# Kernel optimization log

Measured on AMD Instinct MI355X. Metric: run time of the kernel, lower is better.

## Reference

```python
import jax, jax.numpy as jnp
from jax import lax
import numpy as np

DIM = 384
NUM_HEADS = 8
HEAD_DIM = DIM // NUM_HEADS


def setup_inputs() -> dict:
    key = jax.random.key(0)
    k_x, k_qw, k_qb, k_lw, k_lb = jax.random.split(key, 5)
    B, H, W = 2, 64, 64
    N = H * W
    x = jax.random.normal(k_x, (B, N, DIM), dtype=jnp.float32)
    # nn.Linear(dim, 3*dim): weight (3C, C), bias (3C,)
    qkv_w = jax.random.normal(k_qw, (3 * DIM, DIM), dtype=jnp.float32) * (1.0 / np.sqrt(DIM))
    qkv_b = jax.random.normal(k_qb, (3 * DIM,), dtype=jnp.float32) * 0.02
    # nn.Conv2d(dim, dim, 3, padding=1, groups=dim): weight (C, 1, 3, 3), bias (C,)
    lepe_w = jax.random.normal(k_lw, (DIM, 1, 3, 3), dtype=jnp.float32) * (1.0 / 3.0)
    lepe_b = jax.random.normal(k_lb, (DIM,), dtype=jnp.float32) * 0.02
    return {"x": x, "qkv_w": qkv_w, "qkv_b": qkv_b, "lepe_w": lepe_w, "lepe_b": lepe_b, "H": H, "W": W}


def reference(x, qkv_w, qkv_b, lepe_w, lepe_b, H, W):
    B, N, C = x.shape
    hd = C // NUM_HEADS
    scale = hd ** -0.5
    # qkv projection: (B, N, 3C) -> (B, N, 3, heads, head_dim)
    qkv = (jnp.einsum('bnc,oc->bno', x, qkv_w) + qkv_b).reshape(B, N, 3, NUM_HEADS, hd)
    q, k, v = qkv[:, :, 0], qkv[:, :, 1], qkv[:, :, 2]  # each (B, N, heads, hd)
    attn = jnp.einsum('bnhd,bmhd->bhnm', q * scale, k)   # (B, heads, N, N)
    attn = jax.nn.softmax(attn, axis=-1)
    out = jnp.einsum('bhnm,bmhd->bnhd', attn, v).reshape(B, N, C)
    # LePE: depthwise 3x3 conv on v in NCHW layout
    v_img = v.reshape(B, H, W, C).transpose(0, 3, 1, 2)  # (B, C, H, W)
    lepe = lax.conv_general_dilated(
        v_img, lepe_w, window_strides=(1, 1), padding='SAME',
        feature_group_count=C,
        dimension_numbers=('NCHW', 'OIHW', 'NCHW'))
    lepe = lepe + lepe_b[None, :, None, None]
    return out + lepe.transpose(0, 2, 3, 1).reshape(B, N, C)
```

## Files before the change

kernel.cpp:

```cpp
#include <hip/hip_runtime.h>
#include <stdint.h>

#define DIM   384
#define NH    8
#define HD    48
#define NTOK  4096
#define KDIM  384
#define SCALEL2E 0.20823509610f

typedef float  f32x4   __attribute__((ext_vector_type(4)));
typedef float  f32x16  __attribute__((ext_vector_type(16)));
typedef __bf16 bf16x8  __attribute__((ext_vector_type(8)));

#if __has_builtin(__builtin_amdgcn_exp2f)
#define EXP2F(x) __builtin_amdgcn_exp2f(x)
#else
#define EXP2F(x) exp2f(x)
#endif

__device__ __forceinline__ unsigned short f2bf(float f) {
  union { float f; unsigned int u; } c; c.f = f;
  unsigned int r = (c.u + 0x7FFFu + ((c.u >> 16) & 1u)) >> 16;
  return (unsigned short)r;
}
__device__ __forceinline__ float bf2f(unsigned short h) {
  union { unsigned int u; float f; } c; c.u = ((unsigned int)h) << 16;
  return c.f;
}


__global__ void prep_kernel(const float* __restrict__ x, const float* __restrict__ w,
                            unsigned short* __restrict__ x_bf,
                            unsigned short* __restrict__ w_bf) {
  int tid = blockIdx.x * blockDim.x + threadIdx.x;
  int stride = gridDim.x * blockDim.x;
  for (int i = tid; i < 786432; i += stride) {
    float4 v = ((const float4*)x)[i];
    ushort4 o;
    o.x = f2bf(v.x); o.y = f2bf(v.y); o.z = f2bf(v.z); o.w = f2bf(v.w);
    ((ushort4*)x_bf)[i] = o;
  }
  for (int i = tid; i < 110592; i += stride) {
    float4 v = ((const float4*)w)[i];
    ushort4 o;
    o.x = f2bf(v.x); o.y = f2bf(v.y); o.z = f2bf(v.z); o.w = f2bf(v.w);
    ((ushort4*)w_bf)[i] = o;
  }
}

__global__ __launch_bounds__(256) void qkv_gemm(
    const unsigned short* __restrict__ A,
    const unsigned short* __restrict__ Bw,
    const float* __restrict__ bias,
    unsigned short* __restrict__ qc,
    unsigned short* __restrict__ kc,
    unsigned short* __restrict__ v_t) {
  __shared__ unsigned short ldsA[128 * 32];
  __shared__ unsigned short ldsB[64 * 32];
  __shared__ unsigned short ebuf[64 * 72];
  const int tid = threadIdx.x;
  const int wv = tid >> 6, ln = tid & 63;
  const int lrow = ln & 15, lq = ln >> 4;
  const int m0 = blockIdx.x * 128;
  const int n0 = blockIdx.y * 64;
  const int wm = (wv >> 1) * 64, wn = (wv & 1) * 32;

  f32x4 acc[4][2];
#pragma unroll
  for (int mi = 0; mi < 4; ++mi)
#pragma unroll
    for (int ni = 0; ni < 2; ++ni)
#pragma unroll
      for (int r = 0; r < 4; ++r) acc[mi][ni][r] = 0.f;

  for (int k0 = 0; k0 < KDIM; k0 += 32) {
    __syncthreads();
#pragma unroll
    for (int j = 0; j < 2; ++j) {
      int r16 = wv * 2 + j;
      const unsigned short* ga = A + (size_t)(m0 + r16 * 16 + (ln >> 2)) * KDIM
                                   + k0 + (ln & 3) * 8;
      __builtin_amdgcn_global_load_lds(
          (const __attribute__((address_space(1))) void*)ga,
          (__attribute__((address_space(3))) void*)&ldsA[r16 * 512], 16, 0, 0);
    }
    const unsigned short* gb = Bw + (size_t)(n0 + wv * 16 + (ln >> 2)) * KDIM
                                  + k0 + (ln & 3) * 8;
    __builtin_amdgcn_global_load_lds(
        (const __attribute__((address_space(1))) void*)gb,
        (__attribute__((address_space(3))) void*)&ldsB[wv * 512], 16, 0, 0);
    __syncthreads();
    bf16x8 af[4], bfv[2];
#pragma unroll
    for (int mi = 0; mi < 4; ++mi)
      af[mi] = *(const bf16x8*)&ldsA[(wm + mi * 16 + lrow) * 32 + lq * 8];
#pragma unroll
    for (int ni = 0; ni < 2; ++ni)
      bfv[ni] = *(const bf16x8*)&ldsB[(wn + ni * 16 + lrow) * 32 + lq * 8];
#pragma unroll
    for (int mi = 0; mi < 4; ++mi)
#pragma unroll
      for (int ni = 0; ni < 2; ++ni)
        acc[mi][ni] = __builtin_amdgcn_mfma_f32_16x16x32_bf16(
            af[mi], bfv[ni], acc[mi][ni], 0, 0, 0);
  }

  const int region = (n0 >= 768) ? 2 : (n0 >= 384 ? 1 : 0);
  const float scl = (region == 0) ? SCALEL2E : 1.0f;
  const float bias0 = bias[n0 + wn + lrow];
  const float bias1 = bias[n0 + wn + 16 + lrow];

#pragma unroll
  for (int half = 0; half < 2; ++half) {
    __syncthreads();
    if ((wv >> 1) == half) {
#pragma unroll
      for (int mi = 0; mi < 4; ++mi)
#pragma unroll
        for (int ni = 0; ni < 2; ++ni)
#pragma unroll
          for (int r = 0; r < 4; ++r) {
            int row = mi * 16 + lq * 4 + r;
            int col = wn + ni * 16 + lrow;
            float val = (acc[mi][ni][r] + (ni ? bias1 : bias0)) * scl;
            ebuf[row * 72 + col] = f2bf(val);
          }
    }
    __syncthreads();
    if (region < 2) {
      unsigned short* dst = (region == 0) ? qc : kc;
      const int obase = n0 - region * 384;
#pragma unroll
      for (int i = 0; i < 2; ++i) {
        int id = tid + i * 256;
        int row = id >> 3, cc = id & 7;
        uint4 val = *(const uint4*)&ebuf[row * 72 + cc * 8];
        int nrow = m0 + half * 64 + row;
        int b = nrow >> 12, nn = nrow & 4095;
        int o = obase + cc * 8;
        int h = o / 48, d = o - h * 48;
        *(uint4*)&dst[((size_t)(b * 8 + h) * NTOK + nn) * HD + d] = val;
      }
    } else {
#pragma unroll
      for (int i = 0; i < 2; ++i) {
        int id = tid + i * 256;
        int col = id & 63, rc = id >> 6;
        int r0 = rc * 8;
        union { unsigned short s[8]; uint4 u; } pk;
#pragma unroll
        for (int j = 0; j < 8; ++j)
          pk.s[j] = ebuf[(r0 + j) * 72 + col];
        int nrow = m0 + half * 64 + r0;
        int b = nrow >> 12;
        int o = n0 - 768 + col;
        *(uint4*)&v_t[((size_t)(b * DIM + o)) * NTOK + (nrow & 4095)] = pk.u;
      }
    }
  }
}

__global__ __launch_bounds__(256, 4) void attn_kernel(
    const unsigned short* __restrict__ qc,
    const unsigned short* __restrict__ kcg,
    const unsigned short* __restrict__ v_t,
    const float* __restrict__ lw, const float* __restrict__ lb,
    float* __restrict__ out) {
  __shared__ __align__(16) char smem[33280];
  unsigned short* Kl = (unsigned short*)smem;
  unsigned short* Vl = (unsigned short*)(smem + 16384);
  float* Lsum = (float*)(smem + 32768);
  float* Ol   = (float*)smem;

  const int tid = threadIdx.x;
  const int wv = tid >> 6, ln = tid & 63;
  const int kh = wv >> 1;
  const int wq = wv & 1;
  const int l31 = ln & 31, hh = ln >> 5;
  const int th = tid & 127;
  const int qb = blockIdx.x, bh = blockIdx.y;
  const int b = bh >> 3, hd = bh & 7;

  unsigned short* Kh = Kl + kh * 4096;
  unsigned short* Vh = Vl + kh * 4096;

  int kro[3], kgo[3], vro[3], vgo[3];
#pragma unroll
  for (int i = 0; i < 3; ++i) {
    int idx = th + i * 128;
    int r = idx / 6, cc = idx - r * 6;
    kro[i] = r * 64 + ((cc ^ (r & 7)) * 8);
    kgo[i] = r * 48 + cc * 8;
    int vd = idx >> 3, vc = idx & 7;
    vro[i] = vd * 64 + ((vc ^ (vd & 7)) * 8);
    vgo[i] = vd * 4096 + vc * 8;
  }

  if (th < 8) {
    uint4 one4 = make_uint4(0x3F803F80u, 0x3F803F80u, 0x3F803F80u, 0x3F803F80u);
    *(uint4*)&Vh[3072 + th * 8] = one4;
  }

  const int qrb_self = wq * 32 + l31;
  const unsigned short* qp = qc + ((size_t)bh * NTOK + qb * 64 + qrb_self) * HD + hh * 8;
  bf16x8 Qf[3];
#pragma unroll
  for (int hs = 0; hs < 3; ++hs)
    Qf[hs] = *(const bf16x8*)(qp + hs * 16);

  f32x16 Oacc[2];
#pragma unroll
  for (int dc = 0; dc < 2; ++dc)
#pragma unroll
    for (int r = 0; r < 16; ++r) Oacc[dc][r] = 0.f;

  const unsigned short* kbase = kcg + (size_t)bh * NTOK * HD;
  const unsigned short* vbase = v_t + ((size_t)b * DIM + hd * HD) * NTOK;

  for (int it = 0; it < 32; ++it) {
    const int kt = kh * 32 + it;
    __syncthreads();
    const unsigned short* kg = kbase + (size_t)kt * 64 * HD;
    const unsigned short* vg = vbase + kt * 64;
#pragma unroll
    for (int i = 0; i < 3; ++i) {
      *(uint4*)&Kh[kro[i]] = *(const uint4*)(kg + kgo[i]);
      *(uint4*)&Vh[vro[i]] = *(const uint4*)(vg + vgo[i]);
    }
    __syncthreads();

    unsigned int P32[16];
#pragma unroll
    for (int C = 0; C < 2; ++C) {
      f32x16 s;
#pragma unroll
      for (int r = 0; r < 16; ++r) s[r] = 0.f;
      const int krow = C * 32 + l31;
      const unsigned short* kr = &Kh[krow * 64];
      const int rx = krow & 7;
#pragma unroll
      for (int hs = 0; hs < 3; ++hs) {
        bf16x8 kf = *(const bf16x8*)&kr[((hs * 2 + hh) ^ rx) * 8];
        s = __builtin_amdgcn_mfma_f32_32x32x16_bf16(kf, Qf[hs], s, 0, 0, 0);
      }
#pragma unroll
      for (int t8 = 0; t8 < 8; ++t8) {
        float e0 = EXP2F(s[2 * t8]);
        float e1 = EXP2F(s[2 * t8 + 1]);
        P32[C * 8 + t8] = __builtin_amdgcn_perm(
            __float_as_uint(e1), __float_as_uint(e0), 0x07060302u);
      }
    }

#pragma unroll
    for (int s4 = 0; s4 < 4; ++s4) {
      const int o = (s4 >> 1) * 8 + (s4 & 1) * 4;
      unsigned int send1 = hh ? P32[o + 0] : P32[o + 2];
      unsigned int send2 = hh ? P32[o + 1] : P32[o + 3];
      unsigned int recv1 = (unsigned int)__shfl_xor((int)send1, 32, 64);
      unsigned int recv2 = (unsigned int)__shfl_xor((int)send2, 32, 64);
      union { unsigned int u[4]; bf16x8 v; } pa;
      pa.u[0] = hh ? recv1 : P32[o + 0];
      pa.u[1] = hh ? recv2 : P32[o + 1];
      pa.u[2] = hh ? P32[o + 2] : recv1;
      pa.u[3] = hh ? P32[o + 3] : recv2;
#pragma unroll
      for (int dc = 0; dc < 2; ++dc) {
        int vrow = dc * 32 + l31;
        bf16x8 vf = *(const bf16x8*)&Vh[vrow * 64 + (((s4 * 2 + hh) ^ (vrow & 7)) * 8)];
        Oacc[dc] = __builtin_amdgcn_mfma_f32_32x32x16_bf16(pa.v, vf, Oacc[dc], 0, 0, 0);
      }
    }
  }

  __syncthreads();
  if (l31 == 16) {
#pragma unroll
    for (int r = 0; r < 16; ++r) {
      int qrb = wq * 32 + (r & 3) + 8 * (r >> 2) + 4 * hh;
      Lsum[kh * 64 + qrb] = Oacc[1][r];
    }
  }
  {
    const int px = tid & 63;
    const int c0 = (tid >> 6) * 12;
    const int y = qb;
    const unsigned short* vpl = v_t + ((size_t)b * DIM + hd * HD) * NTOK;
    for (int cj = 0; cj < 12; ++cj) {
      int c = c0 + cj;
      const float* wp = lw + (size_t)(hd * HD + c) * 9;
      float a = lb[hd * HD + c];
      const unsigned short* pl = vpl + (size_t)c * NTOK + y * 64 + px;
#pragma unroll
      for (int dy = -1; dy <= 1; ++dy) {
        if ((unsigned)(y + dy) < 64u) {
#pragma unroll
          for (int dx = -1; dx <= 1; ++dx) {
            if ((unsigned)(px + dx) < 64u)
              a += wp[(dy + 1) * 3 + (dx + 1)] * bf2f(pl[dy * 64 + dx]);
          }
        }
      }
      Ol[px * 48 + c] = a;
    }
  }
  __syncthreads();
  if (kh == 1) {
#pragma unroll
    for (int r = 0; r < 16; ++r) {
      int qrb = wq * 32 + (r & 3) + 8 * (r >> 2) + 4 * hh;
      float linv = 1.0f / (Lsum[qrb] + Lsum[64 + qrb]);
      Ol[qrb * 48 + l31] += Oacc[0][r] * linv;
      if (l31 < 16) Ol[qrb * 48 + 32 + l31] += Oacc[1][r] * linv;
    }
  }
  __syncthreads();
  if (kh == 0) {
#pragma unroll
    for (int r = 0; r < 16; ++r) {
      int qrb = wq * 32 + (r & 3) + 8 * (r >> 2) + 4 * hh;
      float linv = 1.0f / (Lsum[qrb] + Lsum[64 + qrb]);
      float* op = out + ((size_t)(b * NTOK + qb * 64 + qrb)) * DIM + hd * HD;
      op[l31] = Ol[qrb * 48 + l31] + Oacc[0][r] * linv;
      if (l31 < 16) op[32 + l31] = Ol[qrb * 48 + 32 + l31] + Oacc[1][r] * linv;
    }
  }
}

extern "C" void kernel_launch(void* const* d_in, const int* in_sizes, int n_in,
                              void* d_out, int out_size, void* d_ws, size_t ws_size,
                              hipStream_t stream) {
  const float* x      = (const float*)d_in[0];
  const float* qkv_w  = (const float*)d_in[1];
  const float* qkv_b  = (const float*)d_in[2];
  const float* lepe_w = (const float*)d_in[3];
  const float* lepe_b = (const float*)d_in[4];

  char* ws = (char*)d_ws;
  unsigned short* x_bf = (unsigned short*)(ws);
  unsigned short* w_bf = (unsigned short*)(ws + 6291456);
  unsigned short* qcp  = (unsigned short*)(ws + 7176192);
  unsigned short* kcp  = (unsigned short*)(ws + 13467648);
  unsigned short* v_t  = (unsigned short*)(ws + 19759104);
  float* out = (float*)d_out;

  prep_kernel<<<1024, 256, 0, stream>>>(x, qkv_w, x_bf, w_bf);
  qkv_gemm<<<dim3(64, 18), 256, 0, stream>>>(x_bf, w_bf, qkv_b, qcp, kcp, v_t);
  attn_kernel<<<dim3(64, 16), 256, 0, stream>>>(qcp, kcp, v_t, lepe_w, lepe_b, out);
}
```

Measured before the change: 213.4 us.

## Split LePE into separate kernel and process 128 queries per attention block

The depthwise LePE convolution moves into its own kernel, which stages v rows with halos in shared memory and writes the result straight to out. The attention kernel then adds its normalized output onto that. Each attention block now handles two 64-query sets, so every K/V tile loaded into shared memory is reused twice. This halves the grid to 512 blocks and doubles the accumulator registers (launch bounds drop to 2 waves per SIMD). It adds a kernel launch and a read-modify-write of out, and it risks lower occupancy and tail effects.

```diff
diff --git a/kernel.cpp b/kernel.cpp
--- a/kernel.cpp
+++ b/kernel.cpp
@@ -160,13 +160,57 @@
   }
 }
 
-__global__ __launch_bounds__(256, 4) void attn_kernel(
+__global__ __launch_bounds__(256) void lepe_kernel(
+    const unsigned short* __restrict__ v_t,
+    const float* __restrict__ lw, const float* __restrict__ lb,
+    float* __restrict__ out) {
+  __shared__ __align__(16) unsigned short pl[16 * 648];
+  const int cg = blockIdx.x;
+  const int sy = blockIdx.y;
+  const int b  = blockIdx.z;
+  const int t = threadIdx.x;
+  const int y0 = sy * 8;
+#pragma unroll
+  for (int i = 0; i < 5; ++i) {
+    int id = t + i * 256;
+    int c = id / 80, rem = id - c * 80;
+    int row = rem >> 3, cx = rem & 7;
+    int y = y0 - 1 + row;
+    uint4 val = make_uint4(0u, 0u, 0u, 0u);
+    if (y >= 0 && y < 64)
+      val = *(const uint4*)(v_t + ((size_t)(b * DIM + cg * 16 + c)) * NTOK + y * 64 + cx * 8);
+    *(uint4*)&pl[c * 648 + row * 64 + cx * 8] = val;
+  }
+  __syncthreads();
+  const int c = t & 15, pg = t >> 4;
+  const int cglob = cg * 16 + c;
+  float w[9];
+#pragma unroll
+  for (int j = 0; j < 9; ++j) w[j] = lw[cglob * 9 + j];
+  const float bias = lb[cglob];
+  const unsigned short* base = &pl[c * 648];
+  for (int i = 0; i < 32; ++i) {
+    int p = pg * 32 + i;
+    int lr = p >> 6, x = p & 63;
+    float acc = bias;
+#pragma unroll
+    for (int ky = 0; ky < 3; ++ky)
+#pragma unroll
+      for (int kx = 0; kx < 3; ++kx) {
+        int xx = x + kx - 1;
+        if (xx >= 0 && xx < 64)
+          acc += w[ky * 3 + kx] * bf2f(base[(lr + ky) * 64 + xx]);
+      }
+    out[((size_t)(b * NTOK + sy * 512 + p)) * DIM + cglob] = acc;
+  }
+}
+
+__global__ __launch_bounds__(256, 2) void attn_kernel(
     const unsigned short* __restrict__ qc,
     const unsigned short* __restrict__ kcg,
     const unsigned short* __restrict__ v_t,
-    const float* __restrict__ lw, const float* __restrict__ lb,
     float* __restrict__ out) {
-  __shared__ __align__(16) char smem[33280];
+  __shared__ __align__(16) char smem[33792];
   unsigned short* Kl = (unsigned short*)smem;
   unsigned short* Vl = (unsigned short*)(smem + 16384);
   float* Lsum = (float*)(smem + 32768);
@@ -178,19 +222,24 @@
   const int wq = wv & 1;
   const int l31 = ln & 31, hh = ln >> 5;
   const int th = tid & 127;
-  const int qb = blockIdx.x, bh = blockIdx.y;
+  const int qb = blockIdx.x;
+  const int bh = blockIdx.y;
   const int b = bh >> 3, hd = bh & 7;
 
   unsigned short* Kh = Kl + kh * 4096;
   unsigned short* Vh = Vl + kh * 4096;
 
-  int kro[3], kgo[3], vro[3], vgo[3];
+  int kro[4], kgo[4], vro[3], vgo[3];
+#pragma unroll
+  for (int i = 0; i < 4; ++i) {
+    int idx = th + i * 128;
+    int r = idx >> 3, cc = idx & 7;
+    kro[i] = r * 64 + ((cc ^ (r & 7)) * 8);
+    kgo[i] = r * 48 + cc * 8;
+  }
 #pragma unroll
   for (int i = 0; i < 3; ++i) {
     int idx = th + i * 128;
-    int r = idx / 6, cc = idx - r * 6;
-    kro[i] = r * 64 + ((cc ^ (r & 7)) * 8);
-    kgo[i] = r * 48 + cc * 8;
     int vd = idx >> 3, vc = idx & 7;
     vro[i] = vd * 64 + ((vc ^ (vd & 7)) * 8);
     vgo[i] = vd * 4096 + vc * 8;
@@ -201,18 +250,23 @@
     *(uint4*)&Vh[3072 + th * 8] = one4;
   }
 
-  const int qrb_self = wq * 32 + l31;
-  const unsigned short* qp = qc + ((size_t)bh * NTOK + qb * 64 + qrb_self) * HD + hh * 8;
-  bf16x8 Qf[3];
-#pragma unroll
-  for (int hs = 0; hs < 3; ++hs)
-    Qf[hs] = *(const bf16x8*)(qp + hs * 16);
-
-  f32x16 Oacc[2];
-#pragma unroll
-  for (int dc = 0; dc < 2; ++dc)
-#pragma unroll
-    for (int r = 0; r < 16; ++r) Oacc[dc][r] = 0.f;
+  bf16x8 Qf[2][3];
+#pragma unroll
+  for (int set = 0; set < 2; ++set) {
+    const int qrow = qb * 128 + set * 64 + wq * 32 + l31;
+    const unsigned short* qp = qc + ((size_t)bh * NTOK + qrow) * HD + hh * 8;
+#pragma unroll
+    for (int hs = 0; hs < 3; ++hs)
+      Qf[set][hs] = *(const bf16x8*)(qp + hs * 16);
+  }
+
+  f32x16 Oacc[2][2];
+#pragma unroll
+  for (int set = 0; set < 2; ++set)
+#pragma unroll
+    for (int dc = 0; dc < 2; ++dc)
+#pragma unroll
+      for (int r = 0; r < 16; ++r) Oacc[set][dc][r] = 0.f;
 
   const unsigned short* kbase = kcg + (size_t)bh * NTOK * HD;
   const unsigned short* vbase = v_t + ((size_t)b * DIM + hd * HD) * NTOK;
@@ -223,52 +277,65 @@
     const unsigned short* kg = kbase + (size_t)kt * 64 * HD;
     const unsigned short* vg = vbase + kt * 64;
 #pragma unroll
-    for (int i = 0; i < 3; ++i) {
+    for (int i = 0; i < 4; ++i)
       *(uint4*)&Kh[kro[i]] = *(const uint4*)(kg + kgo[i]);
+#pragma unroll
+    for (int i = 0; i < 3; ++i)
       *(uint4*)&Vh[vro[i]] = *(const uint4*)(vg + vgo[i]);
-    }
-    __syncthreads();
-
-    unsigned int P32[16];
+    __syncthreads();
+
+    unsigned int P32[2][16];
 #pragma unroll
     for (int C = 0; C < 2; ++C) {
-      f32x16 s;
-#pragma unroll
-      for (int r = 0; r < 16; ++r) s[r] = 0.f;
+      f32x16 sA, sB;
+#pragma unroll
+      for (int r = 0; r < 16; ++r) { sA[r] = 0.f; sB[r] = 0.f; }
       const int krow = C * 32 + l31;
       const unsigned short* kr = &Kh[krow * 64];
       const int rx = krow & 7;
 #pragma unroll
       for (int hs = 0; hs < 3; ++hs) {
         bf16x8 kf = *(const bf16x8*)&kr[((hs * 2 + hh) ^ rx) * 8];
-        s = __builtin_amdgcn_mfma_f32_32x32x16_bf16(kf, Qf[hs], s, 0, 0, 0);
+        sA = __builtin_amdgcn_mfma_f32_32x32x16_bf16(kf, Qf[0][hs], sA, 0, 0, 0);
+        sB = __builtin_amdgcn_mfma_f32_32x32x16_bf16(kf, Qf[1][hs], sB, 0, 0, 0);
       }
 #pragma unroll
       for (int t8 = 0; t8 < 8; ++t8) {
-        float e0 = EXP2F(s[2 * t8]);
-        float e1 = EXP2F(s[2 * t8 + 1]);
-        P32[C * 8 + t8] = __builtin_amdgcn_perm(
-            __float_as_uint(e1), __float_as_uint(e0), 0x07060302u);
+        float a0 = EXP2F(sA[2 * t8]);
+        float a1 = EXP2F(sA[2 * t8 + 1]);
+        P32[0][C * 8 + t8] = __builtin_amdgcn_perm(
+            __float_as_uint(a1), __float_as_uint(a0), 0x07060302u);
+        float b0 = EXP2F(sB[2 * t8]);
+        float b1 = EXP2F(sB[2 * t8 + 1]);
+        P32[1][C * 8 + t8] = __builtin_amdgcn_perm(
+            __float_as_uint(b1), __float_as_uint(b0), 0x07060302u);
       }
     }
 
 #pragma unroll
     for (int s4 = 0; s4 < 4; ++s4) {
-      const int o = (s4 >> 1) * 8 + (s4 & 1) * 4;
-      unsigned int send1 = hh ? P32[o + 0] : P32[o + 2];
-      unsigned int send2 = hh ? P32[o + 1] : P32[o + 3];
-      unsigned int recv1 = (unsigned int)__shfl_xor((int)send1, 32, 64);
-      unsigned int recv2 = (unsigned int)__shfl_xor((int)send2, 32, 64);
-      union { unsigned int u[4]; bf16x8 v; } pa;
-      pa.u[0] = hh ? recv1 : P32[o + 0];
-      pa.u[1] = hh ? recv2 : P32[o + 1];
-      pa.u[2] = hh ? P32[o + 2] : recv1;
-      pa.u[3] = hh ? P32[o + 3] : recv2;
+      bf16x8 vf[2];
 #pragma unroll
       for (int dc = 0; dc < 2; ++dc) {
         int vrow = dc * 32 + l31;
-        bf16x8 vf = *(const bf16x8*)&Vh[vrow * 64 + (((s4 * 2 + hh) ^ (vrow & 7)) * 8)];
-        Oacc[dc] = __builtin_amdgcn_mfma_f32_32x32x16_bf16(pa.v, vf, Oacc[dc], 0, 0, 0);
+        vf[dc] = *(const bf16x8*)&Vh[vrow * 64 + (((s4 * 2 + hh) ^ (vrow & 7)) * 8)];
+      }
+      const int o = (s4 >> 1) * 8 + (s4 & 1) * 4;
+#pragma unroll
+      for (int set = 0; set < 2; ++set) {
+        unsigned int send1 = hh ? P32[set][o + 0] : P32[set][o + 2];
+        unsigned int send2 = hh ? P32[set][o + 1] : P32[set][o + 3];
+        unsigned int recv1 = (unsigned int)__shfl_xor((int)send1, 32, 64);
+        unsigned int recv2 = (unsigned int)__shfl_xor((int)send2, 32, 64);
+        union { unsigned int u[4]; bf16x8 v; } pa;
+        pa.u[0] = hh ? recv1 : P32[set][o + 0];
+        pa.u[1] = hh ? recv2 : P32[set][o + 1];
+        pa.u[2] = hh ? P32[set][o + 2] : recv1;
+        pa.u[3] = hh ? P32[set][o + 3] : recv2;
+#pragma unroll
+        for (int dc = 0; dc < 2; ++dc)
+          Oacc[set][dc] = __builtin_amdgcn_mfma_f32_32x32x16_bf16(
+              pa.v, vf[dc], Oacc[set][dc], 0, 0, 0);
       }
     }
   }
@@ -276,54 +343,36 @@
   __syncthreads();
   if (l31 == 16) {
 #pragma unroll
-    for (int r = 0; r < 16; ++r) {
-      int qrb = wq * 32 + (r & 3) + 8 * (r >> 2) + 4 * hh;
-      Lsum[kh * 64 + qrb] = Oacc[1][r];
-    }
-  }
-  {
-    const int px = tid & 63;
-    const int c0 = (tid >> 6) * 12;
-    const int y = qb;
-    const unsigned short* vpl = v_t + ((size_t)b * DIM + hd * HD) * NTOK;
-    for (int cj = 0; cj < 12; ++cj) {
-      int c = c0 + cj;
-      const float* wp = lw + (size_t)(hd * HD + c) * 9;
-      float a = lb[hd * HD + c];
-      const unsigned short* pl = vpl + (size_t)c * NTOK + y * 64 + px;
-#pragma unroll
-      for (int dy = -1; dy <= 1; ++dy) {
-        if ((unsigned)(y + dy) < 64u) {
-#pragma unroll
-          for (int dx = -1; dx <= 1; ++dx) {
-            if ((unsigned)(px + dx) < 64u)
-              a += wp[(dy + 1) * 3 + (dx + 1)] * bf2f(pl[dy * 64 + dx]);
-          }
-        }
-      }
-      Ol[px * 48 + c] = a;
-    }
-  }
-  __syncthreads();
+    for (int set = 0; set < 2; ++set)
+#pragma unroll
+      for (int r = 0; r < 16; ++r) {
+        int qrb = set * 64 + wq * 32 + (r & 3) + 8 * (r >> 2) + 4 * hh;
+        Lsum[kh * 128 + qrb] = Oacc[set][1][r];
+      }
+  }
   if (kh == 1) {
 #pragma unroll
-    for (int r = 0; r < 16; ++r) {
-      int qrb = wq * 32 + (r & 3) + 8 * (r >> 2) + 4 * hh;
-      float linv = 1.0f / (Lsum[qrb] + Lsum[64 + qrb]);
-      Ol[qrb * 48 + l31] += Oacc[0][r] * linv;
-      if (l31 < 16) Ol[qrb * 48 + 32 + l31] += Oacc[1][r] * linv;
-    }
+    for (int set = 0; set < 2; ++set)
+#pragma unroll
+      for (int r = 0; r < 16; ++r) {
+        int qrb = set * 64 + wq * 32 + (r & 3) + 8 * (r >> 2) + 4 * hh;
+        Ol[qrb * 48 + l31] = Oacc[set][0][r];
+        if (l31 < 16) Ol[qrb * 48 + 32 + l31] = Oacc[set][1][r];
+      }
   }
   __syncthreads();
   if (kh == 0) {
 #pragma unroll
-    for (int r = 0; r < 16; ++r) {
-      int qrb = wq * 32 + (r & 3) + 8 * (r >> 2) + 4 * hh;
-      float linv = 1.0f / (Lsum[qrb] + Lsum[64 + qrb]);
-      float* op = out + ((size_t)(b * NTOK + qb * 64 + qrb)) * DIM + hd * HD;
-      op[l31] = Ol[qrb * 48 + l31] + Oacc[0][r] * linv;
-      if (l31 < 16) op[32 + l31] = Ol[qrb * 48 + 32 + l31] + Oacc[1][r] * linv;
-    }
+    for (int set = 0; set < 2; ++set)
+#pragma unroll
+      for (int r = 0; r < 16; ++r) {
+        int qrb = set * 64 + wq * 32 + (r & 3) + 8 * (r >> 2) + 4 * hh;
+        float linv = 1.0f / (Lsum[qrb] + Lsum[128 + qrb]);
+        float* op = out + ((size_t)(b * NTOK + qb * 128 + qrb)) * DIM + hd * HD;
+        op[l31] += (Oacc[set][0][r] + Ol[qrb * 48 + l31]) * linv;
+        if (l31 < 16)
+          op[32 + l31] += (Oacc[set][1][r] + Ol[qrb * 48 + 32 + l31]) * linv;
+      }
   }
 }
 
@@ -346,5 +395,6 @@
 
   prep_kernel<<<1024, 256, 0, stream>>>(x, qkv_w, x_bf, w_bf);
   qkv_gemm<<<dim3(64, 18), 256, 0, stream>>>(x_bf, w_bf, qkv_b, qcp, kcp, v_t);
-  attn_kernel<<<dim3(64, 16), 256, 0, stream>>>(qcp, kcp, v_t, lepe_w, lepe_b, out);
-}
+  lepe_kernel<<<dim3(24, 8, 2), 256, 0, stream>>>(v_t, lepe_w, lepe_b, out);
+  attn_kernel<<<dim3(32, 16), 256, 0, stream>>>(qcp, kcp, v_t, out);
+}
```

Result: faster. 207.7 us (-2.7%).
